# Kernel optimization log

Hardware: AMD Instinct MI355X
Metric: run time of the kernel (lower is better)

The kernel has to match this reference:

```python
import jax, jax.numpy as jnp
import numpy as np

COST_CLASS = 1.0
COST_BBOX = 5.0
COST_GIOU = 2.0
BS, Q, NUM_CLASSES, T = 16, 900, 92, 256  # T targets per image


def box_cxcywh_to_xyxy(x):
    cx, cy, w, h = x[..., 0], x[..., 1], x[..., 2], x[..., 3]
    return jnp.stack([cx - 0.5 * w, cy - 0.5 * h, cx + 0.5 * w, cy + 0.5 * h], axis=-1)


def generalized_box_iou(b1, b2):
    # b1: [N,4], b2: [M,4] xyxy -> [N,M]
    area1 = (b1[:, 2] - b1[:, 0]) * (b1[:, 3] - b1[:, 1])
    area2 = (b2[:, 2] - b2[:, 0]) * (b2[:, 3] - b2[:, 1])
    lt = jnp.maximum(b1[:, None, :2], b2[None, :, :2])
    rb = jnp.minimum(b1[:, None, 2:], b2[None, :, 2:])
    wh = jnp.clip(rb - lt, 0.0)
    inter = wh[..., 0] * wh[..., 1]
    union = area1[:, None] + area2[None, :] - inter
    iou = inter / union
    lt_e = jnp.minimum(b1[:, None, :2], b2[None, :, :2])
    rb_e = jnp.maximum(b1[:, None, 2:], b2[None, :, 2:])
    wh_e = jnp.clip(rb_e - lt_e, 0.0)
    area = wh_e[..., 0] * wh_e[..., 1]
    return iou - (area - union) / area


def lsa(cost):
    """Jonker-Volgenant style linear sum assignment (minimize). Returns (row_ind, col_ind)
    sorted by row, matching scipy.optimize.linear_sum_assignment semantics for rectangular C."""
    cost = np.asarray(cost, dtype=np.float64)
    transposed = cost.shape[0] > cost.shape[1]
    if transposed:
        cost = cost.T
    n, m = cost.shape  # n <= m
    INF = np.inf
    u = np.zeros(n + 1)
    v = np.zeros(m + 1)
    p = np.zeros(m + 1, dtype=np.int64)  # p[j]: 1-indexed row assigned to col j (0 = free)
    for i in range(1, n + 1):
        p[0] = i
        j0 = 0
        minv = np.full(m + 1, INF)
        way = np.zeros(m + 1, dtype=np.int64)
        used = np.zeros(m + 1, dtype=bool)
        while True:
            used[j0] = True
            i0 = p[j0]
            cur = np.concatenate(([INF], cost[i0 - 1, :] - u[i0] - v[1:]))
            free = ~used
            free[0] = False
            upd = free & (cur < minv)
            minv = np.where(upd, cur, minv)
            way = np.where(upd, j0, way)
            mfree = np.where(free, minv, INF)
            j1 = int(np.argmin(mfree))
            delta = mfree[j1]
            u[p[used]] += delta
            v[used] -= delta
            minv[~used] -= delta
            j0 = j1
            if p[j0] == 0:
                break
        while j0 != 0:
            j1 = way[j0]
            p[j0] = p[j1]
            j0 = j1
    rows = p[1:] - 1
    cols = np.arange(m)
    mask = rows >= 0
    r, c = rows[mask], cols[mask]
    if transposed:
        r, c = c, r
    order = np.argsort(r, kind='stable')
    return r[order], c[order]


def setup_inputs() -> dict:
    key = jax.random.key(0)
    k1, k2, k3, k4 = jax.random.split(key, 4)
    return {
        'pred_logits': jax.random.normal(k1, (BS, Q, NUM_CLASSES), dtype=jnp.float32),
        'pred_boxes': jax.random.uniform(k2, (BS, Q, 4), dtype=jnp.float32),
        'tgt_labels': jax.random.randint(k3, (BS * T,), 0, NUM_CLASSES, dtype=jnp.int64),
        'tgt_bbox': jax.random.uniform(k4, (BS * T, 4), dtype=jnp.float32),
    }


def reference(pred_logits, pred_boxes, tgt_labels, tgt_bbox):
    bs, nq, nc = pred_logits.shape
    out_prob = jax.nn.softmax(pred_logits.reshape(bs * nq, nc), axis=-1)
    out_bbox = pred_boxes.reshape(bs * nq, 4)
    cost_class = -out_prob[:, tgt_labels]                                  # [bs*Q, sumT]
    cost_bbox = jnp.abs(out_bbox[:, None, :] - tgt_bbox[None, :, :]).sum(-1)  # L1 cdist
    cost_giou = -generalized_box_iou(box_cxcywh_to_xyxy(out_bbox), box_cxcywh_to_xyxy(tgt_bbox))
    C = COST_BBOX * cost_bbox + COST_CLASS * cost_class + COST_GIOU * cost_giou
    C = C.reshape(bs, nq, -1)
    t = tgt_bbox.shape[0] // bs
    Cnp = np.asarray(C)
    rows, cols = [], []
    for b in range(bs):  # per-image assignment (mirrors scipy dispatch in the original)
        r, c = lsa(Cnp[b, :, b * t:(b + 1) * t])
        rows.append(r)
        cols.append(c)
    return C, jnp.asarray(np.stack(rows), dtype=jnp.int64), jnp.asarray(np.stack(cols), dtype=jnp.int64)
```

## Files before the change

kernel.cpp:

```cpp
#include <hip/hip_runtime.h>
#include <math.h>
#include <limits.h>

#define BSZ 16
#define NQ  900
#define NCL 92
#define NT  256
#define SUMT (BSZ*NT)
#define MM  NQ
#define NN  NT
#define NSLOT 15
#define QCHUNK 60
#define WAVES 8
#define BLKT (WAVES*64)
#define RING 512
#define ARR_CAP 4000

__global__ __launch_bounds__(256) void prob_kernel(
    const float* __restrict__ logits, float* __restrict__ P) {
#pragma clang fp contract(off)
  const int w = threadIdx.x >> 6, lane = threadIdx.x & 63;
  const int r = blockIdx.x * 4 + w;
  const size_t base = (size_t)r * NCL;
  const float x1 = logits[base + lane];
  const float x2 = (lane + 64 < NCL) ? logits[base + lane + 64] : -INFINITY;
  float m = fmaxf(x1, x2);
  #pragma unroll
  for (int k = 1; k < 64; k <<= 1) m = fmaxf(m, __shfl_xor(m, k));
  const float e1 = expf(x1 - m);
  const float e2 = (lane + 64 < NCL) ? expf(x2 - m) : 0.f;
  float ssum = e1 + e2;
  #pragma unroll
  for (int k = 1; k < 64; k <<= 1) ssum += __shfl_xor(ssum, k);
  P[base + lane] = e1 / ssum;
  if (lane + 64 < NCL) P[base + lane + 64] = e2 / ssum;
}

__global__ __launch_bounds__(256) void cost_kernel2(
    const float* __restrict__ P, const float* __restrict__ boxes,
    const int* __restrict__ labels, const float* __restrict__ tbox,
    float* __restrict__ C) {
#pragma clang fp contract(off)
  const int tid = threadIdx.x;
  const int jt = blockIdx.x * 256 + tid;
  const int b  = blockIdx.z;
  const int q0 = blockIdx.y * QCHUNK;

  __shared__ float sP[QCHUNK * NCL];
  __shared__ float sB[QCHUNK * 4];

  const size_t pbase = (size_t)(b * NQ + q0) * NCL;
  for (int x = tid; x < QCHUNK * NCL; x += 256) sP[x] = P[pbase + x];
  const size_t bbase = (size_t)(b * NQ + q0) * 4;
  if (tid < QCHUNK * 4) sB[tid] = boxes[bbase + tid];

  const float4 tb = ((const float4*)tbox)[jt];
  const int lab = labels[jt];
  const float tx1 = tb.x - 0.5f*tb.z, ty1 = tb.y - 0.5f*tb.w;
  const float tx2 = tb.x + 0.5f*tb.z, ty2 = tb.y + 0.5f*tb.w;
  const float area2 = (tx2 - tx1) * (ty2 - ty1);
  __syncthreads();

  for (int qq = 0; qq < QCHUNK; ++qq) {
    const float cx = sB[qq*4+0], cy = sB[qq*4+1];
    const float w  = sB[qq*4+2], h  = sB[qq*4+3];
    const float cc = -sP[qq*NCL + lab];
    const float bx1 = cx - 0.5f*w, by1 = cy - 0.5f*h;
    const float bx2 = cx + 0.5f*w, by2 = cy + 0.5f*h;
    const float area1 = (bx2 - bx1) * (by2 - by1);
    const float d0 = fabsf(cx - tb.x), d1 = fabsf(cy - tb.y);
    const float d2 = fabsf(w - tb.z),  d3 = fabsf(h - tb.w);
    const float cb = ((d0 + d1) + d2) + d3;
    const float ltx = fmaxf(bx1, tx1), lty = fmaxf(by1, ty1);
    const float rbx = fminf(bx2, tx2), rby = fminf(by2, ty2);
    const float iw = fmaxf(rbx - ltx, 0.f), ih = fmaxf(rby - lty, 0.f);
    const float inter = iw * ih;
    const float uni = (area1 + area2) - inter;
    const float iou = inter / uni;
    const float ex1 = fminf(bx1, tx1), ey1 = fminf(by1, ty1);
    const float ex2 = fmaxf(bx2, tx2), ey2 = fmaxf(by2, ty2);
    const float ew = fmaxf(ex2 - ex1, 0.f), eh = fmaxf(ey2 - ey1, 0.f);
    const float ea = ew * eh;
    const float giou = iou - (ea - uni) / ea;
    C[(size_t)(b*NQ + q0 + qq) * SUMT + jt] = (5.0f*cb + 1.0f*cc) + 2.0f*(-giou);
  }
}

__global__ __launch_bounds__(256) void transpose_kernel(
    const float* __restrict__ C, float* __restrict__ costT,
    unsigned long long* __restrict__ upack) {
  __shared__ float tile[64][65];
  const int b  = blockIdx.z;
  const int q0 = blockIdx.x * 64, t0 = blockIdx.y * 64;
  const int tx = threadIdx.x & 63, ty = threadIdx.x >> 6;
  #pragma unroll
  for (int i = 0; i < 16; ++i) {
    const int qq = ty + i*4;
    const int q = q0 + qq;
    if (q < NQ)
      tile[qq][tx] = C[((size_t)(b*NQ + q))*SUMT + b*NT + t0 + tx];
  }
  __syncthreads();
  #pragma unroll
  for (int i = 0; i < 16; ++i) {
    const int tt = ty + i*4;
    const int q = q0 + tx;
    if (q < NQ)
      costT[((size_t)(b*NT + t0 + tt))*MM + q] = tile[tx][tt];
  }
  if (upack && threadIdx.x < 64) {
    const int nq = (NQ - q0 < 64) ? (NQ - q0) : 64;
    unsigned long long best = ~0ull;
    for (int qq = 0; qq < nq; ++qq) {
      unsigned bts = __float_as_uint(tile[qq][threadIdx.x]);
      bts = (bts & 0x80000000u) ? ~bts : (bts | 0x80000000u);
      const unsigned long long pk =
          ((unsigned long long)bts << 32) | (unsigned)(q0 + qq);
      if (pk < best) best = pk;
    }
    atomicMin(&upack[b * NN + t0 + threadIdx.x], best);
  }
}

__global__ __launch_bounds__(256) void cost_kernel_fb(
    const float* __restrict__ logits, const float* __restrict__ boxes,
    const int* __restrict__ labels, const float* __restrict__ tbox,
    float* __restrict__ C, float* __restrict__ costT) {
#pragma clang fp contract(off)
  const int bq  = blockIdx.x;
  const int b   = bq / NQ;
  const int tid = threadIdx.x;
  __shared__ float lg[NCL];
  __shared__ float red[128];
  if (tid < NCL) lg[tid] = logits[(size_t)bq * NCL + tid];
  __syncthreads();
  if (tid < 128) red[tid] = (tid < NCL) ? lg[tid] : -INFINITY;
  __syncthreads();
  for (int s = 64; s > 0; s >>= 1) { if (tid < s) red[tid] = fmaxf(red[tid], red[tid+s]); __syncthreads(); }
  const float mx = red[0];
  __syncthreads();
  float e = 0.f;
  if (tid < NCL) e = expf(lg[tid] - mx);
  if (tid < 128) red[tid] = e;
  __syncthreads();
  for (int s = 64; s > 0; s >>= 1) { if (tid < s) red[tid] += red[tid+s]; __syncthreads(); }
  const float sm = red[0];
  __syncthreads();
  if (tid < NCL) lg[tid] = e / sm;
  __syncthreads();
  const float cx = boxes[(size_t)bq*4+0], cy = boxes[(size_t)bq*4+1];
  const float w  = boxes[(size_t)bq*4+2], h  = boxes[(size_t)bq*4+3];
  const float bx1 = cx - 0.5f*w, by1 = cy - 0.5f*h;
  const float bx2 = cx + 0.5f*w, by2 = cy + 0.5f*h;
  const float area1 = (bx2 - bx1) * (by2 - by1);
  const int q = bq - b * NQ;
  for (int jt = tid; jt < SUMT; jt += 256) {
    const float4 tb = ((const float4*)tbox)[jt];
    const int lab = labels[jt];
    const float cc = -lg[lab];
    const float d0 = fabsf(cx - tb.x), d1 = fabsf(cy - tb.y);
    const float d2 = fabsf(w - tb.z),  d3 = fabsf(h - tb.w);
    const float cb = ((d0 + d1) + d2) + d3;
    const float tx1 = tb.x - 0.5f*tb.z, ty1 = tb.y - 0.5f*tb.w;
    const float tx2 = tb.x + 0.5f*tb.z, ty2 = tb.y + 0.5f*tb.w;
    const float area2 = (tx2 - tx1) * (ty2 - ty1);
    const float ltx = fmaxf(bx1, tx1), lty = fmaxf(by1, ty1);
    const float rbx = fminf(bx2, tx2), rby = fminf(by2, ty2);
    const float iw = fmaxf(rbx - ltx, 0.f), ih = fmaxf(rby - lty, 0.f);
    const float inter = iw * ih;
    const float uni = (area1 + area2) - inter;
    const float iou = inter / uni;
    const float ex1 = fminf(bx1, tx1), ey1 = fminf(by1, ty1);
    const float ex2 = fmaxf(bx2, tx2), ey2 = fmaxf(by2, ty2);
    const float ew = fmaxf(ex2 - ex1, 0.f), eh = fmaxf(ey2 - ey1, 0.f);
    const float ea = ew * eh;
    const float giou = iou - (ea - uni) / ea;
    const float cval = (5.0f*cb + 1.0f*cc) + 2.0f*(-giou);
    C[(size_t)bq * SUMT + jt] = cval;
    if (costT && (jt >> 8) == b) costT[(size_t)jt * MM + q] = cval;
  }
}

__global__ __launch_bounds__(BLKT) void lsa_kernel(
    const float* __restrict__ C, const float* __restrict__ costT,
    const unsigned long long* __restrict__ upack,
    float* __restrict__ rows_out, float* __restrict__ cols_out) {
  const int b   = blockIdx.x;
  const int tid = threadIdx.x;

  __shared__ double u[NN + 1];
  __shared__ int    p[MM + 1];
  __shared__ int    wayl[MM + 1];
  __shared__ int    claim[MM + 1];
  __shared__ int    rowargmin[NN];
  __shared__ unsigned char rowass[NN];
  __shared__ int    listj[MM + 1];
  __shared__ double listD[MM + 1];
  __shared__ double vs[MM + 1];
  __shared__ int    qring[RING];
  __shared__ int    qhead_sh, qtail_sh, steps_sh;
  __shared__ int    bid_i[WAVES], bid_j[WAVES];
  __shared__ double bid_b1[WAVES], bid_b2[WAVES];

  for (int j = tid; j <= MM; j += BLKT) { p[j] = 0; claim[j] = INT_MAX; vs[j] = 0.0; }
  if (upack) {
    if (tid < NN) {
      const unsigned long long pk = upack[b * NN + tid];
      const unsigned key = (unsigned)(pk >> 32);
      const unsigned bts = (key & 0x80000000u) ? (key & 0x7fffffffu) : ~key;
      u[tid + 1] = (double)__uint_as_float(bts);
      rowargmin[tid] = (int)(pk & 0xffffffffu);
    }
  } else if (costT || C) {
    if (tid < NN) {
      const float* rowptr = C + ((size_t)(b * NQ)) * SUMT + b * NT + tid;
      float mn = INFINITY; int am = 0;
      #pragma unroll 4
      for (int q = 0; q < NQ; ++q) {
        const float cv = rowptr[(size_t)q * SUMT];
        if (cv < mn) { mn = cv; am = q; }
      }
      u[tid + 1] = (double)mn;
      rowargmin[tid] = am;
    }
  }
  if (tid == 0) u[0] = 0.0;
  __syncthreads();
  if (tid < NN) atomicMin(&claim[rowargmin[tid] + 1], tid + 1);
  __syncthreads();
  if (tid < NN) {
    const int am = rowargmin[tid];
    const bool got = (claim[am + 1] == tid + 1);
    rowass[tid] = got ? 1 : 0;
    if (got) p[am + 1] = tid + 1;
  }
  __syncthreads();

  const int lane = tid & 63;
  const int wv   = tid >> 6;
  const float* slab = costT ? costT + (size_t)b * NT * MM : nullptr;

  if (tid < 64) {
    int fcnt = 0;
    #pragma unroll
    for (int c = 0; c < 4; ++c) {
      const bool fr = !rowass[c * 64 + tid];
      const unsigned long long mk = __ballot(fr);
      const int rk = __popcll(mk & ((1ull << tid) - 1ull));
      if (fr) qring[fcnt + rk] = c * 64 + tid + 1;
      fcnt += __popcll(mk);
    }
    if (tid == 0) { qhead_sh = 0; qtail_sh = fcnt; steps_sh = 0; }
  }
  __syncthreads();

  if (slab) {
    while (true) {
      const int head = qhead_sh, tail = qtail_sh, st = steps_sh;
      if (head >= tail || st >= ARR_CAP) break;
      const int nact = ((tail - head) < WAVES) ? (tail - head) : WAVES;

      if (wv < nact) {
        const int i = qring[(head + wv) & (RING - 1)];
        const float* rowp = slab + (size_t)(i - 1) * MM;
        double b1 = INFINITY, b2 = INFINITY; int j1 = MM + 2;
        #pragma unroll
        for (int s = 0; s < NSLOT; ++s) {
          const int j = s * 64 + lane + 1;
          if (j <= MM) {
            const double cand = (double)rowp[j - 1] - vs[j];
            if (cand < b1) { b2 = b1; b1 = cand; j1 = j; }
            else           { b2 = fmin(b2, cand); }
          }
        }
        #pragma unroll
        for (int m = 1; m < 64; m <<= 1) {
          const double ob1 = __shfl_xor(b1, m);
          const double ob2 = __shfl_xor(b2, m);
          const int    oj1 = __shfl_xor(j1, m);
          if (ob1 < b1 || (ob1 == b1 && oj1 < j1)) {
            b2 = fmin(b1, ob2); b1 = ob1; j1 = oj1;
          } else {
            b2 = fmin(b2, ob1);
          }
        }
        if (lane == 0) { bid_i[wv] = i; bid_j[wv] = j1; bid_b1[wv] = b1; bid_b2[wv] = b2; }
      }
      __syncthreads();

      if (tid < nact) {
        const int j1 = bid_j[tid];
        bool dup = false;
        for (int e = 0; e < tid; ++e) if (bid_j[e] == j1) dup = true;
        if (dup) {
          const int slot = atomicAdd(&qtail_sh, 1);
          qring[slot & (RING - 1)] = bid_i[tid];
        } else {
          const double amt = bid_b2[tid] - bid_b1[tid];
          vs[j1] -= amt;
          u[bid_i[tid]] = bid_b2[tid];
          const int k = p[j1];
          p[j1] = bid_i[tid];
          rowass[bid_i[tid] - 1] = 1;
          if (k) {
            rowass[k - 1] = 0;
            const int slot = atomicAdd(&qtail_sh, 1);
            qring[slot & (RING - 1)] = k;
          }
        }
      }
      if (tid == 0) { qhead_sh += nact; steps_sh += nact; }
      __syncthreads();
    }
  }

  if (tid >= 64) return;

  double v_r[NSLOT];
  #pragma unroll
  for (int s = 0; s < NSLOT; ++s) {
    const int j = s * 64 + lane + 1;
    v_r[s] = (j <= MM) ? vs[j] : 0.0;
  }

  for (int ii = 1; ii <= NN; ++ii) {
    if (rowass[ii - 1]) continue;

    double M_r[NSLOT];
    #pragma unroll
    for (int s = 0; s < NSLOT; ++s) M_r[s] = INFINITY;
    unsigned int used = (lane < 4) ? 0u : (1u << 14);
    int    lcount = 0;
    int    j0 = 0;
    double Dsel = 0.0;
    double D = 0.0;
    bool   okrow = true;

    while (true) {
      const int    i0 = (j0 == 0) ? ii : p[j0];
      const double us = u[i0] - Dsel;
      const float* rowp = slab ? slab + (size_t)(i0 - 1) * MM : nullptr;

      double best = INFINITY; int bestj = MM + 2;
      #pragma unroll
      for (int s = 0; s < NSLOT; ++s) {
        if (!(used & (1u << s))) {
          const int j = s * 64 + lane + 1;
          const float cf = rowp ? rowp[j - 1]
              : C[((size_t)(b*NQ + (j-1)))*SUMT + (b*NT + i0 - 1)];
          const double cand = ((double)cf - v_r[s]) - us;
          if (cand < M_r[s]) { M_r[s] = cand; wayl[j] = j0; }
          if (M_r[s] < best) { best = M_r[s]; bestj = j; }
        }
      }
      #pragma unroll
      for (int m = 1; m < 64; m <<= 1) {
        const double ov = __shfl_xor(best, m);
        const int    oj = __shfl_xor(bestj, m);
        if (ov < best || (ov == best && oj < bestj)) { best = ov; bestj = oj; }
      }
      const int j1 = bestj;
      if (j1 > MM) { okrow = false; break; }
      D = best;
      if (lane == ((j1 - 1) & 63)) used |= 1u << ((j1 - 1) >> 6);
      if (p[j1] == 0) { j0 = j1; break; }
      if (lane == 0) { listj[lcount] = j1; listD[lcount] = D; }
      lcount++;
      j0 = j1; Dsel = D;
    }

    if (okrow) {
      for (int e = 0; e < lcount; ++e) {
        const int    je = listj[e];
        const double amt = D - listD[e];
        if (lane == ((je - 1) & 63)) v_r[(je - 1) >> 6] -= amt;
        if (lane == 0) u[p[je]] += amt;
      }
      if (lane == 0) {
        u[ii] += D;
        int jj = j0;
        while (jj) { const int jn = wayl[jj]; const int pn = (jn == 0) ? ii : p[jn]; p[jj] = pn; jj = jn; }
        rowass[ii - 1] = 1;
      }
    }
  }

  int base = 0;
  #pragma unroll
  for (int s = 0; s < NSLOT; ++s) {
    const int j = s * 64 + lane + 1;
    const bool a = (j <= MM) && (p[j] > 0);
    const unsigned long long mask = __ballot(a);
    const int rank = __popcll(mask & ((1ull << lane) - 1ull));
    if (a) {
      rows_out[b*NT + base + rank] = (float)(j - 1);
      cols_out[b*NT + base + rank] = (float)(p[j] - 1);
    }
    base += __popcll(mask);
  }
}

extern "C" void kernel_launch(void* const* d_in, const int* in_sizes, int n_in,
                              void* d_out, int out_size, void* d_ws, size_t ws_size,
                              hipStream_t stream) {
  const float* logits = (const float*)d_in[0];
  const float* boxes  = (const float*)d_in[1];
  const int*   labels = (const int*)d_in[2];
  const float* tbox   = (const float*)d_in[3];

  float* C    = (float*)d_out;
  float* rows = C + (size_t)BSZ * NQ * SUMT;
  float* cols = rows + (size_t)BSZ * NT;

  const size_t needT = (size_t)SUMT * MM * sizeof(float);
  const size_t needP = (size_t)BSZ * NQ * NCL * sizeof(float);
  const size_t needU = (size_t)BSZ * NN * sizeof(unsigned long long);

  if (ws_size >= needP + needT + needU) {
    float* P     = (float*)d_ws;
    float* costT = P + (size_t)BSZ * NQ * NCL;
    unsigned long long* upack = (unsigned long long*)(costT + (size_t)SUMT * MM);
    hipMemsetAsync(upack, 0xFF, needU, stream);
    hipLaunchKernelGGL(prob_kernel, dim3(BSZ*NQ/4), dim3(256), 0, stream, logits, P);
    hipLaunchKernelGGL(cost_kernel2, dim3(SUMT/256, NQ/QCHUNK, BSZ), dim3(256), 0, stream,
                       P, boxes, labels, tbox, C);
    hipLaunchKernelGGL(transpose_kernel, dim3(15, 4, BSZ), dim3(256), 0, stream,
                       C, costT, upack);
    hipLaunchKernelGGL(lsa_kernel, dim3(BSZ), dim3(BLKT), 0, stream,
                       C, costT, upack, rows, cols);
  } else if (ws_size >= needP + needT) {
    float* P     = (float*)d_ws;
    float* costT = P + (size_t)BSZ * NQ * NCL;
    hipLaunchKernelGGL(prob_kernel, dim3(BSZ*NQ/4), dim3(256), 0, stream, logits, P);
    hipLaunchKernelGGL(cost_kernel2, dim3(SUMT/256, NQ/QCHUNK, BSZ), dim3(256), 0, stream,
                       P, boxes, labels, tbox, C);
    hipLaunchKernelGGL(transpose_kernel, dim3(15, 4, BSZ), dim3(256), 0, stream,
                       C, costT, (unsigned long long*)nullptr);
    hipLaunchKernelGGL(lsa_kernel, dim3(BSZ), dim3(BLKT), 0, stream,
                       C, costT, (const unsigned long long*)nullptr, rows, cols);
  } else if (ws_size >= needT) {
    float* costT = (float*)d_ws;
    hipLaunchKernelGGL(cost_kernel_fb, dim3(BSZ*NQ), dim3(256), 0, stream,
                       logits, boxes, labels, tbox, C, costT);
    hipLaunchKernelGGL(lsa_kernel, dim3(BSZ), dim3(BLKT), 0, stream,
                       C, costT, (const unsigned long long*)nullptr, rows, cols);
  } else {
    hipLaunchKernelGGL(cost_kernel_fb, dim3(BSZ*NQ), dim3(256), 0, stream,
                       logits, boxes, labels, tbox, C, (float*)nullptr);
    hipLaunchKernelGGL(lsa_kernel, dim3(BSZ), dim3(BLKT), 0, stream,
                       C, (float*)nullptr, (const unsigned long long*)nullptr, rows, cols);
  }
}
```

Measured before the change: 407.7 us.

## Fuse transpose and column-min into cost kernel; double LSA block waves

Drops the separate transpose kernel. Diagonal blocks of the cost kernel now write the per-image transposed cost rows and do the packed column-minimum atomics directly. This avoids a launch and the re-read of the diagonal C blocks. The transposed writes are strided per thread (one row of MM per thread), so coalescing may be poor. The LSA kernel block size is also doubled from 8 to 16 waves, which raises parallelism within each image's assignment at the cost of heavier block synchronisation.

```diff
diff --git a/kernel.cpp b/kernel.cpp
--- a/kernel.cpp
+++ b/kernel.cpp
@@ -11,7 +11,7 @@
 #define NN  NT
 #define NSLOT 15
 #define QCHUNK 60
-#define WAVES 8
+#define WAVES 16
 #define BLKT (WAVES*64)
 #define RING 512
 #define ARR_CAP 4000
@@ -39,12 +39,14 @@
 __global__ __launch_bounds__(256) void cost_kernel2(
     const float* __restrict__ P, const float* __restrict__ boxes,
     const int* __restrict__ labels, const float* __restrict__ tbox,
-    float* __restrict__ C) {
+    float* __restrict__ C, float* __restrict__ costT,
+    unsigned long long* __restrict__ upack) {
 #pragma clang fp contract(off)
   const int tid = threadIdx.x;
   const int jt = blockIdx.x * 256 + tid;
   const int b  = blockIdx.z;
   const int q0 = blockIdx.y * QCHUNK;
+  const bool diag = (blockIdx.x == b) && (costT != nullptr);
 
   __shared__ float sP[QCHUNK * NCL];
   __shared__ float sB[QCHUNK * 4];
@@ -60,6 +62,9 @@
   const float tx2 = tb.x + 0.5f*tb.z, ty2 = tb.y + 0.5f*tb.w;
   const float area2 = (tx2 - tx1) * (ty2 - ty1);
   __syncthreads();
+
+  float* tr = diag ? (costT + ((size_t)(b * NT + tid)) * MM + q0) : nullptr;
+  unsigned long long best = ~0ull;
 
   for (int qq = 0; qq < QCHUNK; ++qq) {
     const float cx = sB[qq*4+0], cy = sB[qq*4+1];
@@ -82,44 +87,18 @@
     const float ew = fmaxf(ex2 - ex1, 0.f), eh = fmaxf(ey2 - ey1, 0.f);
     const float ea = ew * eh;
     const float giou = iou - (ea - uni) / ea;
-    C[(size_t)(b*NQ + q0 + qq) * SUMT + jt] = (5.0f*cb + 1.0f*cc) + 2.0f*(-giou);
-  }
-}
-
-__global__ __launch_bounds__(256) void transpose_kernel(
-    const float* __restrict__ C, float* __restrict__ costT,
-    unsigned long long* __restrict__ upack) {
-  __shared__ float tile[64][65];
-  const int b  = blockIdx.z;
-  const int q0 = blockIdx.x * 64, t0 = blockIdx.y * 64;
-  const int tx = threadIdx.x & 63, ty = threadIdx.x >> 6;
-  #pragma unroll
-  for (int i = 0; i < 16; ++i) {
-    const int qq = ty + i*4;
-    const int q = q0 + qq;
-    if (q < NQ)
-      tile[qq][tx] = C[((size_t)(b*NQ + q))*SUMT + b*NT + t0 + tx];
-  }
-  __syncthreads();
-  #pragma unroll
-  for (int i = 0; i < 16; ++i) {
-    const int tt = ty + i*4;
-    const int q = q0 + tx;
-    if (q < NQ)
-      costT[((size_t)(b*NT + t0 + tt))*MM + q] = tile[tx][tt];
-  }
-  if (upack && threadIdx.x < 64) {
-    const int nq = (NQ - q0 < 64) ? (NQ - q0) : 64;
-    unsigned long long best = ~0ull;
-    for (int qq = 0; qq < nq; ++qq) {
-      unsigned bts = __float_as_uint(tile[qq][threadIdx.x]);
+    const float cval = (5.0f*cb + 1.0f*cc) + 2.0f*(-giou);
+    C[(size_t)(b*NQ + q0 + qq) * SUMT + jt] = cval;
+    if (diag) {
+      tr[qq] = cval;
+      unsigned bts = __float_as_uint(cval);
       bts = (bts & 0x80000000u) ? ~bts : (bts | 0x80000000u);
       const unsigned long long pk =
           ((unsigned long long)bts << 32) | (unsigned)(q0 + qq);
       if (pk < best) best = pk;
     }
-    atomicMin(&upack[b * NN + t0 + threadIdx.x], best);
-  }
+  }
+  if (diag && upack) atomicMin(&upack[b * NN + tid], best);
 }
 
 __global__ __launch_bounds__(256) void cost_kernel_fb(
@@ -423,9 +402,7 @@
     hipMemsetAsync(upack, 0xFF, needU, stream);
     hipLaunchKernelGGL(prob_kernel, dim3(BSZ*NQ/4), dim3(256), 0, stream, logits, P);
     hipLaunchKernelGGL(cost_kernel2, dim3(SUMT/256, NQ/QCHUNK, BSZ), dim3(256), 0, stream,
-                       P, boxes, labels, tbox, C);
-    hipLaunchKernelGGL(transpose_kernel, dim3(15, 4, BSZ), dim3(256), 0, stream,
-                       C, costT, upack);
+                       P, boxes, labels, tbox, C, costT, upack);
     hipLaunchKernelGGL(lsa_kernel, dim3(BSZ), dim3(BLKT), 0, stream,
                        C, costT, upack, rows, cols);
   } else if (ws_size >= needP + needT) {
@@ -433,9 +410,7 @@
     float* costT = P + (size_t)BSZ * NQ * NCL;
     hipLaunchKernelGGL(prob_kernel, dim3(BSZ*NQ/4), dim3(256), 0, stream, logits, P);
     hipLaunchKernelGGL(cost_kernel2, dim3(SUMT/256, NQ/QCHUNK, BSZ), dim3(256), 0, stream,
-                       P, boxes, labels, tbox, C);
-    hipLaunchKernelGGL(transpose_kernel, dim3(15, 4, BSZ), dim3(256), 0, stream,
-                       C, costT, (unsigned long long*)nullptr);
+                       P, boxes, labels, tbox, C, costT, (unsigned long long*)nullptr);
     hipLaunchKernelGGL(lsa_kernel, dim3(BSZ), dim3(BLKT), 0, stream,
                        C, costT, (const unsigned long long*)nullptr, rows, cols);
   } else if (ws_size >= needT) {
```

After: 388.7 us. 1.05x faster.
